# Kernel tuning notes

Hardware: AMD Instinct MI355X
Metric: run time of the kernel (lower is better)

Reference implementation:

```python
import jax, jax.numpy as jnp
import numpy as np

N = 1024  # codeword length (power of 2)
K = 512   # info bits
BATCH = 65536
NB_STAGES = int(np.log2(N))  # 10


def _gen_indices(n):
    """Stage-wise gather indices; index n points at a sentinel zero column."""
    nb_stages = int(np.log2(n))
    ind_gather = np.full((nb_stages, n + 1), n, dtype=np.int32)
    for s in range(nb_stages):
        ind_range = np.arange(n // 2)
        ind_dest = ind_range * 2 - np.mod(ind_range, 2 ** s)
        ind_gather[s, ind_dest] = ind_dest + 2 ** s
    return ind_gather


def setup_inputs() -> dict:
    key = jax.random.key(0)
    # binary information bits, float32 as in the original layer
    u = jax.random.randint(key, (BATCH, K), 0, 2).astype(jnp.float32)
    frozen_pos = np.arange(N - K)
    info_pos = jnp.asarray(np.setdiff1d(np.arange(N), frozen_pos), dtype=jnp.int32)  # [K]
    ind_gather = jnp.asarray(_gen_indices(N))  # [NB_STAGES, N+1]
    return {"u": u, "info_pos": info_pos, "ind_gather": ind_gather}


def reference(u, info_pos, ind_gather) -> jnp.ndarray:
    b = u.shape[0]
    # scatter info bits into codeword positions; frozen positions stay 0
    c = jnp.zeros((b, N), u.dtype).at[:, info_pos].set(u)
    # append sentinel zero column at index N (gather target for pass-through lanes)
    x = jnp.concatenate([c, jnp.zeros((b, 1), u.dtype)], axis=1)  # [b, N+1]
    # log2(N)-stage butterfly: XOR == add mod 2 for binary values
    for s in range(NB_STAGES):
        x = jnp.mod(x + x[:, ind_gather[s]], 2.0)
    return x[:, :N]
```

## Files before the change

### kernel.cpp

```cpp
#include <hip/hip_runtime.h>


#define PN     1024
#define PK     512
#define PBATCH 65536
#define WORDS  32

__global__ __launch_bounds__(256) void build_inv_kernel(
    const int* __restrict__ info_pos, int* __restrict__ inv)
{
    const int tid = threadIdx.x;
    #pragma unroll
    for (int i = tid; i < PN; i += 256) inv[i] = -1;
    __syncthreads();
    #pragma unroll
    for (int k = tid; k < PK; k += 256) inv[info_pos[k]] = k;
}

__global__ __launch_bounds__(256) void polar_encode_kernel(
    const float* __restrict__ u,
    const int*   __restrict__ ginv,
    float*       __restrict__ out)
{
    __shared__ float su[4][2 * PK];

    const int tid  = threadIdx.x;
    const int lane = tid & 63;
    const int wave = tid >> 6;
    const int l31  = lane & 31;
    const int half = lane >> 5;
    const unsigned rA = blockIdx.x * 8u + wave * 2u;

    const float4* u4 = (const float4*)(u + (size_t)rA * PK);
    const float4 r0 = u4[       lane];
    const float4 r1 = u4[ 64 + lane];
    const float4 r2 = u4[128 + lane];
    const float4 r3 = u4[192 + lane];

    float4* su4 = (float4*)su[wave];
    su4[       lane] = r0;
    su4[ 64 + lane] = r1;
    su4[128 + lane] = r2;
    su4[192 + lane] = r3;

    const float* srow = su[wave] + half * PK;
    unsigned int word = 0;
    #pragma unroll
    for (int c = 0; c < WORDS; ++c) {
        const int   iv  = ginv[c * 32 + l31];
        const float v   = srow[iv & (PK - 1)];
        const bool  bit = (iv >= 0) && (v != 0.0f);
        const unsigned long long m = __ballot(bit);
        const unsigned int sel =
            half ? (unsigned int)(m >> 32) : (unsigned int)m;
        if (l31 == c) word = sel;
    }

    word ^= (word >> 1)  & 0x55555555u;
    word ^= (word >> 2)  & 0x33333333u;
    word ^= (word >> 4)  & 0x0F0F0F0Fu;
    word ^= (word >> 8)  & 0x00FF00FFu;
    word ^= (word >> 16) & 0x0000FFFFu;

    #pragma unroll
    for (int off = 1; off <= 16; off <<= 1) {
        const unsigned int partner =
            (unsigned int)__shfl_xor((int)word, off, 64);
        if ((l31 & off) == 0) word ^= partner;
    }

    float4* out4 = (float4*)out;
    const unsigned base = rA * (PN / 4);
    #pragma unroll
    for (int j = 0; j < 8; ++j) {
        const int f   = j * 64 + lane;
        const int r   = f >> 8;
        const int wir = (f & 255) >> 3;
        const int src = wir + (r << 5);
        const unsigned int b   = (unsigned int)__shfl((int)word, src, 64);
        const unsigned int nib = (b >> ((lane & 7) * 4)) & 0xFu;
        float4 v4;
        v4.x = (nib & 1u) ? 1.0f : 0.0f;
        v4.y = (nib & 2u) ? 1.0f : 0.0f;
        v4.z = (nib & 4u) ? 1.0f : 0.0f;
        v4.w = (nib & 8u) ? 1.0f : 0.0f;
        out4[base + f] = v4;
    }
}

extern "C" void kernel_launch(void* const* d_in, const int* in_sizes, int n_in,
                              void* d_out, int out_size, void* d_ws, size_t ws_size,
                              hipStream_t stream) {
    const float* u        = (const float*)d_in[0];
    const int*   info_pos = (const int*)d_in[1];
    float* out = (float*)d_out;
    int*   inv = (int*)d_ws;

    build_inv_kernel<<<1, 256, 0, stream>>>(info_pos, inv);
    polar_encode_kernel<<<PBATCH / 8, 256, 0, stream>>>(u, inv, out);
}
```

Before: 361.2 us.

## Split encoder into bit-pack and streaming expand kernels with nontemporal stores

The encoder now writes packed 32-bit codeword words to workspace. A separate grid-strided kernel expands them into float outputs using nontemporal vector stores. This decouples the compute-heavy pack phase from the write-bandwidth-bound expansion and is meant to improve store streaming. It adds an extra launch and a small intermediate buffer round trip. A fused fallback that builds the inverse map in shared memory is used when the workspace is too small.

Measured after the change: 373.7 us. 3.5% more time.

```diff
diff --git a/kernel.cpp b/kernel.cpp
--- a/kernel.cpp
+++ b/kernel.cpp
@@ -5,6 +5,10 @@
 #define PK     512
 #define PBATCH 65536
 #define WORDS  32
+#define TOTAL_WORDS (PBATCH * WORDS)
+#define TOTAL_F4    (PBATCH * (PN/4))
+
+typedef float vf4 __attribute__((ext_vector_type(4)));
 
 __global__ __launch_bounds__(256) void build_inv_kernel(
     const int* __restrict__ info_pos, int* __restrict__ inv)
@@ -17,10 +21,10 @@
     for (int k = tid; k < PK; k += 256) inv[info_pos[k]] = k;
 }
 
-__global__ __launch_bounds__(256) void polar_encode_kernel(
+__global__ __launch_bounds__(256) void polar_pack_kernel(
     const float* __restrict__ u,
     const int*   __restrict__ ginv,
-    float*       __restrict__ out)
+    unsigned int* __restrict__ wout)
 {
     __shared__ float su[4][2 * PK];
 
@@ -36,7 +40,6 @@
     const float4 r1 = u4[ 64 + lane];
     const float4 r2 = u4[128 + lane];
     const float4 r3 = u4[192 + lane];
-
     float4* su4 = (float4*)su[wave];
     su4[       lane] = r0;
     su4[ 64 + lane] = r1;
@@ -69,6 +72,77 @@
         if ((l31 & off) == 0) word ^= partner;
     }
 
+    wout[rA * WORDS + lane] = word;
+}
+
+__global__ __launch_bounds__(256) void polar_expand_kernel(
+    const unsigned int* __restrict__ words,
+    vf4* __restrict__ out4)
+{
+    const unsigned stride = gridDim.x * 256u;
+    unsigned f = blockIdx.x * 256u + threadIdx.x;
+    #pragma unroll
+    for (int i = 0; i < 8; ++i, f += stride) {
+        const unsigned int w   = words[f >> 3];
+        const unsigned int nib = (w >> ((f & 7u) * 4u)) & 0xFu;
+        vf4 v;
+        v.x = (nib & 1u) ? 1.0f : 0.0f;
+        v.y = (nib & 2u) ? 1.0f : 0.0f;
+        v.z = (nib & 4u) ? 1.0f : 0.0f;
+        v.w = (nib & 8u) ? 1.0f : 0.0f;
+        __builtin_nontemporal_store(v, out4 + f);
+    }
+}
+
+__global__ __launch_bounds__(256) void polar_fused_kernel(
+    const float* __restrict__ u,
+    const int*   __restrict__ info_pos,
+    float*       __restrict__ out)
+{
+    __shared__ int   inv[PN];
+    __shared__ float su[4][2 * PK];
+    const int tid = threadIdx.x;
+    #pragma unroll
+    for (int i = tid; i < PN; i += 256) inv[i] = -1;
+    __syncthreads();
+    #pragma unroll
+    for (int k = tid; k < PK; k += 256) inv[info_pos[k]] = k;
+    __syncthreads();
+
+    const int lane = tid & 63;
+    const int wave = tid >> 6;
+    const int l31  = lane & 31;
+    const int half = lane >> 5;
+    const unsigned rA = blockIdx.x * 8u + wave * 2u;
+
+    const float4* u4 = (const float4*)(u + (size_t)rA * PK);
+    float4* su4 = (float4*)su[wave];
+    #pragma unroll
+    for (int j = 0; j < 4; ++j) su4[j * 64 + lane] = u4[j * 64 + lane];
+
+    const float* srow = su[wave] + half * PK;
+    unsigned int word = 0;
+    #pragma unroll
+    for (int c = 0; c < WORDS; ++c) {
+        const int   iv  = inv[c * 32 + l31];
+        const float v   = srow[iv & (PK - 1)];
+        const bool  bit = (iv >= 0) && (v != 0.0f);
+        const unsigned long long m = __ballot(bit);
+        const unsigned int sel =
+            half ? (unsigned int)(m >> 32) : (unsigned int)m;
+        if (l31 == c) word = sel;
+    }
+    word ^= (word >> 1)  & 0x55555555u;
+    word ^= (word >> 2)  & 0x33333333u;
+    word ^= (word >> 4)  & 0x0F0F0F0Fu;
+    word ^= (word >> 8)  & 0x00FF00FFu;
+    word ^= (word >> 16) & 0x0000FFFFu;
+    #pragma unroll
+    for (int off = 1; off <= 16; off <<= 1) {
+        const unsigned int partner =
+            (unsigned int)__shfl_xor((int)word, off, 64);
+        if ((l31 & off) == 0) word ^= partner;
+    }
     float4* out4 = (float4*)out;
     const unsigned base = rA * (PN / 4);
     #pragma unroll
@@ -94,8 +168,17 @@
     const float* u        = (const float*)d_in[0];
     const int*   info_pos = (const int*)d_in[1];
     float* out = (float*)d_out;
-    int*   inv = (int*)d_ws;
 
-    build_inv_kernel<<<1, 256, 0, stream>>>(info_pos, inv);
-    polar_encode_kernel<<<PBATCH / 8, 256, 0, stream>>>(u, inv, out);
+    const size_t need = (size_t)PN * 4 + (size_t)TOTAL_WORDS * 4;
+    if (ws_size >= need) {
+        int*          inv   = (int*)d_ws;
+        unsigned int* words = (unsigned int*)((char*)d_ws + PN * 4);
+
+        build_inv_kernel<<<1, 256, 0, stream>>>(info_pos, inv);
+        polar_pack_kernel<<<PBATCH / 8, 256, 0, stream>>>(u, inv, words);
+        polar_expand_kernel<<<TOTAL_F4 / (8 * 256), 256, 0, stream>>>(
+            words, (vf4*)out);
+    } else {
+        polar_fused_kernel<<<PBATCH / 8, 256, 0, stream>>>(u, info_pos, out);
+    }
 }
```
